# Kernel optimization log

Hardware: AMD Instinct MI355X
Metric: run time of the kernel (lower is better)

## Reference

```python
import jax, jax.numpy as jnp
import numpy as np

B, N, C = 8, 4096, 512

def setup_inputs() -> dict:
    key = jax.random.key(0)
    k1, k2, k3, k4, k5, k6 = jax.random.split(key, 6)
    x = jax.random.normal(k1, (B, N, C), dtype=jnp.float32)
    adj = jax.random.uniform(k2, (B, C, C), dtype=jnp.float32)
    # params: stored [in, out] so y = x @ W + b (equivalent to torch Linear)
    s = 1.0 / np.sqrt(C)
    Wqkv = jax.random.uniform(k3, (C, 3 * C), dtype=jnp.float32, minval=-s, maxval=s)
    bqkv = jax.random.uniform(k4, (3 * C,), dtype=jnp.float32, minval=-s, maxval=s)
    Wo = jax.random.uniform(k5, (C, C), dtype=jnp.float32, minval=-s, maxval=s)
    bo = jax.random.uniform(k6, (C,), dtype=jnp.float32, minval=-s, maxval=s)
    return {"x": x, "adj": adj, "Wqkv": Wqkv, "bqkv": bqkv, "Wo": Wo, "bo": bo}

def reference(x, adj, Wqkv, bqkv, Wo, bo):
    # qkv projection + ReLU gating
    qkv = jnp.einsum('bnc,cd->bnd', x, Wqkv) + bqkv          # [B,N,3C]
    q, k, v = jnp.split(qkv, 3, axis=-1)                      # each [B,N,C]
    q, k, v = jax.nn.relu(q), jax.nn.relu(k), jax.nn.relu(v)
    dk = q.shape[-1]
    # channel-wise scores: q^T k over tokens -> [B,C,C]
    scores = jnp.einsum('bnc,bnd->bcd', q, k) / jnp.sqrt(jnp.float32(dk))
    attn = jax.nn.softmax(scores, axis=-1)
    attn = attn * adj                                         # post-softmax adjacency gate
    y = jnp.einsum('bnc,bcd->bnd', v, attn)                   # value.matmul(attention)
    return jnp.einsum('bnc,cd->bnd', y, Wo) + bo
```

## Files before the change

kernel.cpp:

```cpp
#include <hip/hip_runtime.h>

#define B_ 8
#define N_ 4096
#define C_ 512

typedef _Float16 f16;
typedef __attribute__((ext_vector_type(8))) _Float16 f16x8;
typedef __attribute__((ext_vector_type(4))) _Float16 f16x4;
typedef __attribute__((ext_vector_type(4))) float f32x4;

#define GLL16(gsrc, ldst)                                                      \
  __builtin_amdgcn_global_load_lds(                                            \
      (const __attribute__((address_space(1))) void*)(gsrc),                   \
      (__attribute__((address_space(3))) void*)(ldst), 16, 0, 0)

__device__ __forceinline__ int xcd_remap(int bid, int nwg) {
  return (bid & 7) * (nwg >> 3) + (bid >> 3);
}

template <int LDA2, int LDB2, int NT>
__device__ __forceinline__ void mainloop32(const char* __restrict__ Agb,
                                           const char* __restrict__ Bgb,
                                           f16* Als, f16* Bls,
                                           f32x4 (&acc)[4][4]) {
  const int tid = threadIdx.x;
  const int lane = tid & 63;
  const int wv = tid >> 6;
  const int wr = wv >> 1;
  const int wc = wv & 1;

  const int r15 = lane & 15;
  const int g8 = (lane >> 4) << 3;
  const int swz = (r15 & 3) << 3;
  const int kx = g8 ^ swz;
  const int awbase = (wr * 64 + r15) * 32;
  const int bwbase = (wc * 64 + r15) * 32;

  int rowl[2], colb[2];
#pragma unroll
  for (int ld = 0; ld < 2; ++ld) {
    const int doff = (ld * 256 + tid) * 16;
    rowl[ld] = doff >> 6;
    colb[ld] = (doff & 63) ^ ((rowl[ld] & 3) << 4);
  }

  auto stage = [&](int t) {
    if (t >= NT) return;
    f16* la = Als + (t & 1) * 4096 + wv * 512;
    f16* lb = Bls + (t & 1) * 4096 + wv * 512;
#pragma unroll
    for (int ld = 0; ld < 2; ++ld) {
      GLL16(Agb + (size_t)rowl[ld] * LDA2 + (size_t)t * 64 + colb[ld],
            la + ld * 2048);
      GLL16(Bgb + (size_t)rowl[ld] * LDB2 + (size_t)t * 64 + colb[ld],
            lb + ld * 2048);
    }
  };

  stage(0);
  __syncthreads();

  for (int T = 0; T < NT; ++T) {
    stage(T + 1);
    const f16* Ab = Als + (T & 1) * 4096;
    const f16* Bb = Bls + (T & 1) * 4096;
    f16x8 af[4], bf[4];
#pragma unroll
    for (int m = 0; m < 4; ++m)
      af[m] = *(const f16x8*)(Ab + awbase + m * 512 + kx);
#pragma unroll
    for (int n = 0; n < 4; ++n)
      bf[n] = *(const f16x8*)(Bb + bwbase + n * 512 + kx);
#pragma unroll
    for (int m = 0; m < 4; ++m)
#pragma unroll
      for (int n = 0; n < 4; ++n)
        acc[m][n] = __builtin_amdgcn_mfma_f32_16x16x32_f16(af[m], bf[n],
                                                           acc[m][n], 0, 0, 0);
    __syncthreads();
  }
}

#define ZERO_ACC(acc)                                                          \
  f32x4 acc[4][4];                                                             \
  _Pragma("unroll") for (int zi = 0; zi < 4; ++zi)                             \
      _Pragma("unroll") for (int zj = 0; zj < 4; ++zj) {                       \
    f32x4 z = {0.f, 0.f, 0.f, 0.f};                                            \
    acc[zi][zj] = z;                                                           \
  }

__global__ void __launch_bounds__(256) k_cvt_x(const float* __restrict__ in,
                                               f16* __restrict__ out) {
  const int i = blockIdx.x * 256 + threadIdx.x;
  float4 v = ((const float4*)in)[i];
  f16x4 h = {(f16)v.x, (f16)v.y, (f16)v.z, (f16)v.w};
  ((f16x4*)out)[i] = h;
}

__global__ void __launch_bounds__(256) k_transpose_w(const float* __restrict__ w,
                                                     f16* __restrict__ wt,
                                                     int cols) {
  const int idx = blockIdx.x * 256 + threadIdx.x;
  const int n = idx >> 9;
  const int c = idx & 511;
  wt[idx] = (f16)w[(size_t)c * cols + n];
}

__global__ void __launch_bounds__(256, 4)
    k_gemm_qkv(const f16* __restrict__ x16, const f16* __restrict__ wqkvt,
               const float* __restrict__ bqkv, f16* __restrict__ q_t,
               f16* __restrict__ k_t, f16* __restrict__ v16) {
  __shared__ alignas(16) f16 Als[2 * 4096];
  __shared__ alignas(16) f16 Bls[2 * 4096];
  const int l = xcd_remap(blockIdx.x, 3072);
  const int bx = l % 12;
  const int my = l / 12;
  const char* Agb = (const char*)(x16 + (size_t)my * 128 * C_);
  const char* Bgb = (const char*)(wqkvt + (size_t)bx * 128 * C_);
  ZERO_ACC(acc);
  mainloop32<C_ * 2, C_ * 2, C_ / 32>(Agb, Bgb, Als, Bls, acc);

  const int lane = threadIdx.x & 63, wv = threadIdx.x >> 6;
  const int wr = wv >> 1, wc = wv & 1;
  const int sec = bx >> 2;
  const int colbase = bx * 128 + wc * 64;
  const int rowbase = my * 128 + wr * 64;
  const int b = rowbase >> 12;
#pragma unroll
  for (int n = 0; n < 4; ++n) {
    const int col = colbase + n * 16 + (lane & 15);
    const int cch = col & 511;
    const float bias = bqkv[col];
#pragma unroll
    for (int m = 0; m < 4; ++m) {
      const int rg = rowbase + m * 16 + ((lane >> 4) << 2);
      const int nloc = rg & 4095;
      f32x4 a = acc[m][n];
      f16x4 h = {(f16)fmaxf(a[0] + bias, 0.f), (f16)fmaxf(a[1] + bias, 0.f),
                 (f16)fmaxf(a[2] + bias, 0.f), (f16)fmaxf(a[3] + bias, 0.f)};
      if (sec == 0) {
        *(f16x4*)(q_t + ((size_t)b * C_ + cch) * N_ + nloc) = h;
      } else if (sec == 1) {
        *(f16x4*)(k_t + ((size_t)b * C_ + cch) * N_ + nloc) = h;
      } else {
        f16* dst = v16 + (size_t)rg * C_ + cch;
        dst[0] = h[0];
        dst[C_] = h[1];
        dst[2 * C_] = h[2];
        dst[3 * C_] = h[3];
      }
    }
  }
}

__global__ void __launch_bounds__(256, 4)
    k_gemm_scores(const f16* __restrict__ q_t, const f16* __restrict__ k_t,
                  f16* __restrict__ spart) {
  __shared__ alignas(16) f16 Als[2 * 4096];
  __shared__ alignas(16) f16 Bls[2 * 4096];
  const int l = xcd_remap(blockIdx.x, 1024);
  const int bx = l & 3;
  const int by = (l >> 2) & 3;
  const int z = l >> 4;
  const int b = z >> 3, sp = z & 7;
  const char* Agb = (const char*)(q_t + (size_t)b * C_ * N_ +
                                  (size_t)(by * 128) * N_ + sp * 512);
  const char* Bgb = (const char*)(k_t + (size_t)b * C_ * N_ +
                                  (size_t)(bx * 128) * N_ + sp * 512);
  ZERO_ACC(acc);
  mainloop32<N_ * 2, N_ * 2, 16>(Agb, Bgb, Als, Bls, acc);

  const int lane = threadIdx.x & 63, wv = threadIdx.x >> 6;
  const int wr = wv >> 1, wc = wv & 1;
  f16* base = spart + (size_t)(sp * B_ + b) * C_ * C_;
#pragma unroll
  for (int n = 0; n < 4; ++n) {
    const int d = bx * 128 + wc * 64 + n * 16 + (lane & 15);
#pragma unroll
    for (int m = 0; m < 4; ++m) {
      const int c0 = by * 128 + wr * 64 + m * 16 + ((lane >> 4) << 2);
#pragma unroll
      for (int r = 0; r < 4; ++r)
        base[(size_t)(c0 + r) * C_ + d] = (f16)acc[m][n][r];
    }
  }
}

__global__ void __launch_bounds__(256)
    k_softmax_gate(const f16* __restrict__ spart,
                   const float* __restrict__ adj, f16* __restrict__ attn) {
  const int wv = threadIdx.x >> 6, lane = threadIdx.x & 63;
  const int row = blockIdx.x * 4 + wv;
  const size_t ro = (size_t)row * 512;
  const int off = lane * 8;

  float s[8] = {0.f, 0.f, 0.f, 0.f, 0.f, 0.f, 0.f, 0.f};
#pragma unroll
  for (int sp = 0; sp < 8; ++sp) {
    f16x8 v = *(const f16x8*)(spart + (size_t)sp * (B_ * C_ * C_) + ro + off);
#pragma unroll
    for (int i = 0; i < 8; ++i) s[i] += (float)v[i];
  }
  const float scale = 0.044194173824159216f;
  float mx = -1e30f;
#pragma unroll
  for (int i = 0; i < 8; ++i) {
    s[i] *= scale;
    mx = fmaxf(mx, s[i]);
  }
#pragma unroll
  for (int d = 32; d > 0; d >>= 1) mx = fmaxf(mx, __shfl_xor(mx, d, 64));
  float e[8], sum = 0.f;
#pragma unroll
  for (int i = 0; i < 8; ++i) {
    e[i] = __expf(s[i] - mx);
    sum += e[i];
  }
#pragma unroll
  for (int d = 32; d > 0; d >>= 1) sum += __shfl_xor(sum, d, 64);
  const float inv = 1.0f / sum;
  const float4 a0 = *(const float4*)(adj + ro + off);
  const float4 a1 = *(const float4*)(adj + ro + off + 4);
  f16x8 o;
  o[0] = (f16)(e[0] * inv * a0.x); o[1] = (f16)(e[1] * inv * a0.y);
  o[2] = (f16)(e[2] * inv * a0.z); o[3] = (f16)(e[3] * inv * a0.w);
  o[4] = (f16)(e[4] * inv * a1.x); o[5] = (f16)(e[5] * inv * a1.y);
  o[6] = (f16)(e[6] * inv * a1.z); o[7] = (f16)(e[7] * inv * a1.w);
  *(f16x8*)(attn + ro + off) = o;
}

__global__ void __launch_bounds__(256)
    k_gemm_m(const f16* __restrict__ attn, const f16* __restrict__ wot,
             f16* __restrict__ mt) {
  __shared__ alignas(16) f16 Als[2 * 4096];
  __shared__ alignas(16) f16 Bls[2 * 4096];
  const int b = blockIdx.z;
  const char* Agb = (const char*)(attn + (size_t)b * C_ * C_ +
                                  (size_t)blockIdx.y * 128 * C_);
  const char* Bgb = (const char*)(wot + (size_t)blockIdx.x * 128 * C_);
  ZERO_ACC(acc);
  mainloop32<C_ * 2, C_ * 2, 16>(Agb, Bgb, Als, Bls, acc);

  const int lane = threadIdx.x & 63, wv = threadIdx.x >> 6;
  const int wr = wv >> 1, wc = wv & 1;
  f16* base = mt + (size_t)b * C_ * C_;
  const int colbase = blockIdx.x * 128 + wc * 64;
  const int rowbase = blockIdx.y * 128 + wr * 64;
#pragma unroll
  for (int j = 0; j < 4; ++j) {
    const int e = colbase + j * 16 + (lane & 15);
#pragma unroll
    for (int i = 0; i < 4; ++i) {
      const int c0 = rowbase + i * 16 + ((lane >> 4) << 2);
      f32x4 a = acc[i][j];
      f16x4 h = {(f16)a[0], (f16)a[1], (f16)a[2], (f16)a[3]};
      *(f16x4*)(base + (size_t)e * C_ + c0) = h;
    }
  }
}

__global__ void __launch_bounds__(256, 4)
    k_gemm_out(const f16* __restrict__ v16, const f16* __restrict__ mt,
               const float* __restrict__ bo, float* __restrict__ out) {
  __shared__ alignas(16) f16 Als[2 * 4096];
  __shared__ alignas(16) f16 Bls[2 * 4096];
  const int l = xcd_remap(blockIdx.x, 1024);
  const int bx = l & 3;
  const int my = l >> 2;
  const int b = (my * 128) >> 12;
  const char* Agb = (const char*)(v16 + (size_t)my * 128 * C_);
  const char* Bgb = (const char*)(mt + (size_t)b * C_ * C_ +
                                  (size_t)(bx * 128) * C_);
  ZERO_ACC(acc);
  mainloop32<C_ * 2, C_ * 2, 16>(Agb, Bgb, Als, Bls, acc);

  const int lane = threadIdx.x & 63, wv = threadIdx.x >> 6;
  const int wr = wv >> 1, wc = wv & 1;
#pragma unroll
  for (int n = 0; n < 4; ++n) {
    const int e = bx * 128 + wc * 64 + n * 16 + (lane & 15);
    const float bias = bo[e];
#pragma unroll
    for (int m = 0; m < 4; ++m) {
      const int rg = my * 128 + wr * 64 + m * 16 + ((lane >> 4) << 2);
#pragma unroll
      for (int r = 0; r < 4; ++r)
        out[(size_t)(rg + r) * C_ + e] = acc[m][n][r] + bias;
    }
  }
}

extern "C" void kernel_launch(void* const* d_in, const int* in_sizes, int n_in,
                              void* d_out, int out_size, void* d_ws,
                              size_t ws_size, hipStream_t stream) {
  const float* x = (const float*)d_in[0];
  const float* adj = (const float*)d_in[1];
  const float* Wqkv = (const float*)d_in[2];
  const float* bqkv = (const float*)d_in[3];
  const float* Wo = (const float*)d_in[4];
  const float* bo = (const float*)d_in[5];
  float* out = (float*)d_out;

  char* ws = (char*)d_ws;
  size_t off = 0;
  auto carve = [&](size_t bytes) -> char* {
    char* p = ws + off;
    off += (bytes + 255) & ~(size_t)255;
    return p;
  };
  f16* x16 = (f16*)carve((size_t)B_ * N_ * C_ * 2);
  f16* wqkvt = (f16*)carve((size_t)3 * C_ * C_ * 2);
  f16* wot = (f16*)carve((size_t)C_ * C_ * 2);
  f16* q_t = (f16*)carve((size_t)B_ * C_ * N_ * 2);
  f16* k_t = (f16*)carve((size_t)B_ * C_ * N_ * 2);
  f16* v16 = (f16*)carve((size_t)B_ * N_ * C_ * 2);
  f16* spart = x16;
  f16* attn16 = k_t;
  f16* mt16 = q_t;

  k_cvt_x<<<(B_ * N_ * C_ / 4) / 256, 256, 0, stream>>>(x, x16);
  k_transpose_w<<<(C_ * 3 * C_) / 256, 256, 0, stream>>>(Wqkv, wqkvt, 3 * C_);
  k_transpose_w<<<(C_ * C_) / 256, 256, 0, stream>>>(Wo, wot, C_);
  k_gemm_qkv<<<3072, 256, 0, stream>>>(x16, wqkvt, bqkv, q_t, k_t, v16);
  k_gemm_scores<<<1024, 256, 0, stream>>>(q_t, k_t, spart);
  k_softmax_gate<<<1024, 256, 0, stream>>>(spart, adj, attn16);
  k_gemm_m<<<dim3(4, 4, B_), 256, 0, stream>>>(attn16, wot, mt16);
  k_gemm_out<<<1024, 256, 0, stream>>>(v16, mt16, bo, out);
}
```

Baseline: 185.7 us.

## Double GEMM K-tile to 64, fuse prep kernels, remap gemm_m blocks

The shared GEMM mainloop now stages a 64-wide K slice per iteration instead of 32, with a wider 8-row XOR swizzle, twice the LDS buffers and two MFMA sub-steps per barrier. This halves the number of barrier/load rounds per GEMM, but the larger LDS footprint lowers the occupancy hint from 4 to 2 blocks per CU. The three input conversion and transpose kernels are merged into one launch, and k_gemm_m uses a 1D grid with XCD remapping.

```diff
diff --git a/kernel.cpp b/kernel.cpp
--- a/kernel.cpp
+++ b/kernel.cpp
@@ -19,10 +19,10 @@
 }
 
 template <int LDA2, int LDB2, int NT>
-__device__ __forceinline__ void mainloop32(const char* __restrict__ Agb,
-                                           const char* __restrict__ Bgb,
-                                           f16* Als, f16* Bls,
-                                           f32x4 (&acc)[4][4]) {
+__device__ __forceinline__ void mainloop2(const char* __restrict__ Agb,
+                                          const char* __restrict__ Bgb,
+                                          f16* Als, f16* Bls,
+                                          f32x4 (&acc)[4][4]) {
   const int tid = threadIdx.x;
   const int lane = tid & 63;
   const int wv = tid >> 6;
@@ -30,29 +30,30 @@
   const int wc = wv & 1;
 
   const int r15 = lane & 15;
-  const int g8 = (lane >> 4) << 3;
-  const int swz = (r15 & 3) << 3;
-  const int kx = g8 ^ swz;
-  const int awbase = (wr * 64 + r15) * 32;
-  const int bwbase = (wc * 64 + r15) * 32;
-
-  int rowl[2], colb[2];
-#pragma unroll
-  for (int ld = 0; ld < 2; ++ld) {
+  const int kc8 = (lane >> 4) << 3;
+  const int swz = (r15 & 7) << 3;
+  const int k0x = kc8 ^ swz;
+  const int k1x = (kc8 + 32) ^ swz;
+  const int awbase = (wr * 64 + r15) * 64;
+  const int bwbase = (wc * 64 + r15) * 64;
+
+  int rowl[4], colb[4];
+#pragma unroll
+  for (int ld = 0; ld < 4; ++ld) {
     const int doff = (ld * 256 + tid) * 16;
-    rowl[ld] = doff >> 6;
-    colb[ld] = (doff & 63) ^ ((rowl[ld] & 3) << 4);
+    rowl[ld] = doff >> 7;
+    colb[ld] = (doff & 127) ^ ((rowl[ld] & 7) << 4);
   }
 
   auto stage = [&](int t) {
     if (t >= NT) return;
-    f16* la = Als + (t & 1) * 4096 + wv * 512;
-    f16* lb = Bls + (t & 1) * 4096 + wv * 512;
-#pragma unroll
-    for (int ld = 0; ld < 2; ++ld) {
-      GLL16(Agb + (size_t)rowl[ld] * LDA2 + (size_t)t * 64 + colb[ld],
+    f16* la = Als + (t & 1) * 8192 + wv * 512;
+    f16* lb = Bls + (t & 1) * 8192 + wv * 512;
+#pragma unroll
+    for (int ld = 0; ld < 4; ++ld) {
+      GLL16(Agb + (size_t)rowl[ld] * LDA2 + (size_t)t * 128 + colb[ld],
             la + ld * 2048);
-      GLL16(Bgb + (size_t)rowl[ld] * LDB2 + (size_t)t * 64 + colb[ld],
+      GLL16(Bgb + (size_t)rowl[ld] * LDB2 + (size_t)t * 128 + colb[ld],
             lb + ld * 2048);
     }
   };
@@ -62,21 +63,27 @@
 
   for (int T = 0; T < NT; ++T) {
     stage(T + 1);
-    const f16* Ab = Als + (T & 1) * 4096;
-    const f16* Bb = Bls + (T & 1) * 4096;
-    f16x8 af[4], bf[4];
-#pragma unroll
-    for (int m = 0; m < 4; ++m)
-      af[m] = *(const f16x8*)(Ab + awbase + m * 512 + kx);
-#pragma unroll
-    for (int n = 0; n < 4; ++n)
-      bf[n] = *(const f16x8*)(Bb + bwbase + n * 512 + kx);
-#pragma unroll
-    for (int m = 0; m < 4; ++m)
-#pragma unroll
-      for (int n = 0; n < 4; ++n)
-        acc[m][n] = __builtin_amdgcn_mfma_f32_16x16x32_f16(af[m], bf[n],
-                                                           acc[m][n], 0, 0, 0);
+    const f16* Ab = Als + (T & 1) * 8192;
+    const f16* Bb = Bls + (T & 1) * 8192;
+    f16x8 af[4][2], bf[4][2];
+#pragma unroll
+    for (int m = 0; m < 4; ++m) {
+      af[m][0] = *(const f16x8*)(Ab + awbase + m * 1024 + k0x);
+      af[m][1] = *(const f16x8*)(Ab + awbase + m * 1024 + k1x);
+    }
+#pragma unroll
+    for (int n = 0; n < 4; ++n) {
+      bf[n][0] = *(const f16x8*)(Bb + bwbase + n * 1024 + k0x);
+      bf[n][1] = *(const f16x8*)(Bb + bwbase + n * 1024 + k1x);
+    }
+#pragma unroll
+    for (int s = 0; s < 2; ++s)
+#pragma unroll
+      for (int m = 0; m < 4; ++m)
+#pragma unroll
+        for (int n = 0; n < 4; ++n)
+          acc[m][n] = __builtin_amdgcn_mfma_f32_16x16x32_f16(
+              af[m][s], bf[n][s], acc[m][n], 0, 0, 0);
     __syncthreads();
   }
 }
@@ -89,36 +96,40 @@
     acc[zi][zj] = z;                                                           \
   }
 
-__global__ void __launch_bounds__(256) k_cvt_x(const float* __restrict__ in,
-                                               f16* __restrict__ out) {
-  const int i = blockIdx.x * 256 + threadIdx.x;
-  float4 v = ((const float4*)in)[i];
-  f16x4 h = {(f16)v.x, (f16)v.y, (f16)v.z, (f16)v.w};
-  ((f16x4*)out)[i] = h;
-}
-
-__global__ void __launch_bounds__(256) k_transpose_w(const float* __restrict__ w,
-                                                     f16* __restrict__ wt,
-                                                     int cols) {
-  const int idx = blockIdx.x * 256 + threadIdx.x;
-  const int n = idx >> 9;
-  const int c = idx & 511;
-  wt[idx] = (f16)w[(size_t)c * cols + n];
-}
-
-__global__ void __launch_bounds__(256, 4)
+__global__ void __launch_bounds__(256)
+    k_prep(const float* __restrict__ x, const float* __restrict__ Wqkv,
+           const float* __restrict__ Wo, f16* __restrict__ x16,
+           f16* __restrict__ wqkvt, f16* __restrict__ wot) {
+  const int bid = blockIdx.x;
+  if (bid < 16384) {
+    const int i = bid * 256 + threadIdx.x;
+    float4 v = ((const float4*)x)[i];
+    f16x4 h = {(f16)v.x, (f16)v.y, (f16)v.z, (f16)v.w};
+    ((f16x4*)x16)[i] = h;
+  } else if (bid < 19456) {
+    const int idx = (bid - 16384) * 256 + threadIdx.x;
+    const int n = idx >> 9, c = idx & 511;
+    wqkvt[idx] = (f16)Wqkv[(size_t)c * 1536 + n];
+  } else {
+    const int idx = (bid - 19456) * 256 + threadIdx.x;
+    const int n = idx >> 9, c = idx & 511;
+    wot[idx] = (f16)Wo[(size_t)c * 512 + n];
+  }
+}
+
+__global__ void __launch_bounds__(256, 2)
     k_gemm_qkv(const f16* __restrict__ x16, const f16* __restrict__ wqkvt,
                const float* __restrict__ bqkv, f16* __restrict__ q_t,
                f16* __restrict__ k_t, f16* __restrict__ v16) {
-  __shared__ alignas(16) f16 Als[2 * 4096];
-  __shared__ alignas(16) f16 Bls[2 * 4096];
+  __shared__ alignas(16) f16 Als[2 * 8192];
+  __shared__ alignas(16) f16 Bls[2 * 8192];
   const int l = xcd_remap(blockIdx.x, 3072);
   const int bx = l % 12;
   const int my = l / 12;
   const char* Agb = (const char*)(x16 + (size_t)my * 128 * C_);
   const char* Bgb = (const char*)(wqkvt + (size_t)bx * 128 * C_);
   ZERO_ACC(acc);
-  mainloop32<C_ * 2, C_ * 2, C_ / 32>(Agb, Bgb, Als, Bls, acc);
+  mainloop2<C_ * 2, C_ * 2, C_ / 64>(Agb, Bgb, Als, Bls, acc);
 
   const int lane = threadIdx.x & 63, wv = threadIdx.x >> 6;
   const int wr = wv >> 1, wc = wv & 1;
@@ -153,11 +164,11 @@
   }
 }
 
-__global__ void __launch_bounds__(256, 4)
+__global__ void __launch_bounds__(256, 2)
     k_gemm_scores(const f16* __restrict__ q_t, const f16* __restrict__ k_t,
                   f16* __restrict__ spart) {
-  __shared__ alignas(16) f16 Als[2 * 4096];
-  __shared__ alignas(16) f16 Bls[2 * 4096];
+  __shared__ alignas(16) f16 Als[2 * 8192];
+  __shared__ alignas(16) f16 Bls[2 * 8192];
   const int l = xcd_remap(blockIdx.x, 1024);
   const int bx = l & 3;
   const int by = (l >> 2) & 3;
@@ -168,7 +179,7 @@
   const char* Bgb = (const char*)(k_t + (size_t)b * C_ * N_ +
                                   (size_t)(bx * 128) * N_ + sp * 512);
   ZERO_ACC(acc);
-  mainloop32<N_ * 2, N_ * 2, 16>(Agb, Bgb, Als, Bls, acc);
+  mainloop2<N_ * 2, N_ * 2, 8>(Agb, Bgb, Als, Bls, acc);
 
   const int lane = threadIdx.x & 63, wv = threadIdx.x >> 6;
   const int wr = wv >> 1, wc = wv & 1;
@@ -229,23 +240,26 @@
   *(f16x8*)(attn + ro + off) = o;
 }
 
-__global__ void __launch_bounds__(256)
+__global__ void __launch_bounds__(256, 2)
     k_gemm_m(const f16* __restrict__ attn, const f16* __restrict__ wot,
              f16* __restrict__ mt) {
-  __shared__ alignas(16) f16 Als[2 * 4096];
-  __shared__ alignas(16) f16 Bls[2 * 4096];
-  const int b = blockIdx.z;
+  __shared__ alignas(16) f16 Als[2 * 8192];
+  __shared__ alignas(16) f16 Bls[2 * 8192];
+  const int l = xcd_remap(blockIdx.x, 128);
+  const int bx = l & 3;
+  const int by = (l >> 2) & 3;
+  const int b = l >> 4;
   const char* Agb = (const char*)(attn + (size_t)b * C_ * C_ +
-                                  (size_t)blockIdx.y * 128 * C_);
-  const char* Bgb = (const char*)(wot + (size_t)blockIdx.x * 128 * C_);
+                                  (size_t)(by * 128) * C_);
+  const char* Bgb = (const char*)(wot + (size_t)(bx * 128) * C_);
   ZERO_ACC(acc);
-  mainloop32<C_ * 2, C_ * 2, 16>(Agb, Bgb, Als, Bls, acc);
+  mainloop2<C_ * 2, C_ * 2, 8>(Agb, Bgb, Als, Bls, acc);
 
   const int lane = threadIdx.x & 63, wv = threadIdx.x >> 6;
   const int wr = wv >> 1, wc = wv & 1;
   f16* base = mt + (size_t)b * C_ * C_;
-  const int colbase = blockIdx.x * 128 + wc * 64;
-  const int rowbase = blockIdx.y * 128 + wr * 64;
+  const int colbase = bx * 128 + wc * 64;
+  const int rowbase = by * 128 + wr * 64;
 #pragma unroll
   for (int j = 0; j < 4; ++j) {
     const int e = colbase + j * 16 + (lane & 15);
@@ -259,11 +273,11 @@
   }
 }
 
-__global__ void __launch_bounds__(256, 4)
+__global__ void __launch_bounds__(256, 2)
     k_gemm_out(const f16* __restrict__ v16, const f16* __restrict__ mt,
                const float* __restrict__ bo, float* __restrict__ out) {
-  __shared__ alignas(16) f16 Als[2 * 4096];
-  __shared__ alignas(16) f16 Bls[2 * 4096];
+  __shared__ alignas(16) f16 Als[2 * 8192];
+  __shared__ alignas(16) f16 Bls[2 * 8192];
   const int l = xcd_remap(blockIdx.x, 1024);
   const int bx = l & 3;
   const int my = l >> 2;
@@ -272,7 +286,7 @@
   const char* Bgb = (const char*)(mt + (size_t)b * C_ * C_ +
                                   (size_t)(bx * 128) * C_);
   ZERO_ACC(acc);
-  mainloop32<C_ * 2, C_ * 2, 16>(Agb, Bgb, Als, Bls, acc);
+  mainloop2<C_ * 2, C_ * 2, 8>(Agb, Bgb, Als, Bls, acc);
 
   const int lane = threadIdx.x & 63, wv = threadIdx.x >> 6;
   const int wr = wv >> 1, wc = wv & 1;
@@ -318,12 +332,10 @@
   f16* attn16 = k_t;
   f16* mt16 = q_t;
 
-  k_cvt_x<<<(B_ * N_ * C_ / 4) / 256, 256, 0, stream>>>(x, x16);
-  k_transpose_w<<<(C_ * 3 * C_) / 256, 256, 0, stream>>>(Wqkv, wqkvt, 3 * C_);
-  k_transpose_w<<<(C_ * C_) / 256, 256, 0, stream>>>(Wo, wot, C_);
+  k_prep<<<20480, 256, 0, stream>>>(x, Wqkv, Wo, x16, wqkvt, wot);
   k_gemm_qkv<<<3072, 256, 0, stream>>>(x16, wqkvt, bqkv, q_t, k_t, v16);
   k_gemm_scores<<<1024, 256, 0, stream>>>(q_t, k_t, spart);
   k_softmax_gate<<<1024, 256, 0, stream>>>(spart, adj, attn16);
-  k_gemm_m<<<dim3(4, 4, B_), 256, 0, stream>>>(attn16, wot, mt16);
+  k_gemm_m<<<128, 256, 0, stream>>>(attn16, wot, mt16);
   k_gemm_out<<<1024, 256, 0, stream>>>(v16, mt16, bo, out);
 }
```

Measured after the change: 169.9 us. 8.5% less time.
